# Optimization experiments

Measured on AMD Instinct MI355X. Metric: run time of the kernel, lower is better.

The kernel has to match this reference:

```python
import jax, jax.numpy as jnp
import numpy as np

N_NODES = 50000
N_EDGES = 800000
ND = 64
ED = 32
MSG = 128
HID = 256
N_AGENTS = 25000


def setup_inputs() -> dict:
    key = jax.random.key(0)
    ks = jax.random.split(key, 12)
    s = lambda k, shape, fan: jax.random.normal(k, shape, jnp.float32) / np.sqrt(fan)
    return {
        'node_feats': jax.random.normal(ks[0], (N_NODES, ND), jnp.float32),
        'edge_feats': jax.random.normal(ks[1], (N_EDGES, ED), jnp.float32),
        'W_msg1': s(ks[2], (2 * ND + ED, HID), 2 * ND + ED),
        'b_msg1': jnp.zeros((HID,), jnp.float32),
        'W_msg2': s(ks[3], (HID, MSG), HID),
        'b_msg2': jnp.zeros((MSG,), jnp.float32),
        'w_gate': s(ks[4], (MSG, 1), MSG),
        'b_gate': jnp.zeros((1,), jnp.float32),
        'W_h1': s(ks[5], (MSG, HID), MSG),
        'b_h1': jnp.zeros((HID,), jnp.float32),
        'W_h2': s(ks[6], (HID, HID), HID),
        'b_h2': jnp.zeros((HID,), jnp.float32),
        'W_out': s(ks[7], (HID, 1), HID),
        'b_out': jnp.zeros((1,), jnp.float32),
        'senders': jax.random.randint(ks[8], (N_EDGES,), 0, N_NODES, jnp.int32),
        'receivers': jax.random.randint(ks[9], (N_EDGES,), 0, N_NODES, jnp.int32),
        'n_agents': N_AGENTS,
    }


def reference(node_feats, edge_feats, W_msg1, b_msg1, W_msg2, b_msg2,
              w_gate, b_gate, W_h1, b_h1, W_h2, b_h2, W_out, b_out,
              senders, receivers, n_agents):
    n_nodes = node_feats.shape[0]
    # gather sender/receiver features, build edge messages (gather-transform)
    msg_in = jnp.concatenate(
        [node_feats[senders], node_feats[receivers], edge_feats], axis=-1)  # [E, 2*ND+ED]
    h = jax.nn.relu(msg_in @ W_msg1 + b_msg1)                               # [E, HID]
    msg = jax.nn.relu(h @ W_msg2 + b_msg2)                                  # [E, MSG]
    # per-receiver segment softmax attention
    logits = (msg @ w_gate + b_gate)[:, 0]                                  # [E]
    seg_max = jax.ops.segment_max(logits, receivers, num_segments=n_nodes)  # [N]
    e = jnp.exp(logits - seg_max[receivers])                                # [E]
    denom = jax.ops.segment_sum(e, receivers, num_segments=n_nodes)         # [N]
    attn = e / (denom[receivers] + 1e-9)                                    # [E]
    # scatter-aggregate messages to nodes
    aggr = jax.ops.segment_sum(attn[:, None] * msg, receivers,
                               num_segments=n_nodes)                        # [N, MSG]
    # node_type == 0: agent nodes are the first n_agents nodes
    x = aggr[:n_agents]                                                     # [A, MSG]
    # head MLP
    x = jax.nn.relu(x @ W_h1 + b_h1)
    x = jax.nn.relu(x @ W_h2 + b_h2)
    # Dense(1) + tanh
    return jnp.tanh(x @ W_out + b_out)                                      # [A, 1]
```

## Files before the change

### kernel.cpp

```cpp
#include <hip/hip_runtime.h>
#include <hip/hip_bf16.h>

#define N_NODES  50000
#define N_EDGES  800000
#define ND       64
#define ED       32
#define MSGD     128
#define HIDD     256
#define N_AGENTS 25000
#define EPAD     800064

typedef _Float16 f16;
typedef __attribute__((ext_vector_type(4))) _Float16 f16x4;
typedef __attribute__((ext_vector_type(8))) _Float16 f16x8;
typedef __attribute__((ext_vector_type(4))) float f32x4;
typedef unsigned short u16;
typedef unsigned int   u32;
typedef unsigned long long u64;

__global__ __launch_bounds__(256) void pack_weights(
    const float* __restrict__ W1, const float* __restrict__ W2,
    const float* __restrict__ Wh1, const float* __restrict__ Wh2,
    f16* __restrict__ F1, f16* __restrict__ F2,
    f16* __restrict__ F3, f16* __restrict__ F4)
{
    int tid  = blockIdx.x * 256 + threadIdx.x;
    int grp  = tid >> 6, lane = tid & 63;
    const float* W; f16* D; int NT, stride, gl;
    if      (grp < 80)  { W = W1;  D = F1; NT = 16; stride = 256; gl = grp; }
    else if (grp < 144) { W = W2;  D = F2; NT = 8;  stride = 128; gl = grp - 80; }
    else if (grp < 208) { W = Wh1; D = F3; NT = 16; stride = 256; gl = grp - 144; }
    else if (grp < 336) { W = Wh2; D = F4; NT = 16; stride = 256; gl = grp - 208; }
    else return;
    int ks = gl / NT, nt = gl - ks * NT;
    int n  = nt * 16 + (lane & 15);
    int k0 = ks * 32 + (lane >> 4) * 8;
    f16* dst = D + ((size_t)gl * 64 + lane) * 8;
    #pragma unroll
    for (int j = 0; j < 8; ++j)
        dst[j] = (f16)W[(size_t)(k0 + j) * stride + n];
}

__global__ __launch_bounds__(256) void compact_kernel(
    const int* __restrict__ recv, const float* __restrict__ nf,
    f16* __restrict__ nf16, int* __restrict__ rankb,
    int* __restrict__ deg)
{
    int i = blockIdx.x * 256 + threadIdx.x;
    {
        float4 v = ((const float4*)nf)[i];
        f16x4 h;
        h.x = (f16)v.x; h.y = (f16)v.y; h.z = (f16)v.z; h.w = (f16)v.w;
        ((f16x4*)nf16)[i] = h;
    }
    int r = recv[i];
    if (r < N_AGENTS)
        rankb[i] = atomicAdd(&deg[r], 1);
}

__global__ __launch_bounds__(1024) void prefix_kernel(
    const int* __restrict__ deg, int* __restrict__ off)
{
    __shared__ int part[1024];
    int t = threadIdx.x;
    int i0 = t * 25;
    int s = 0;
    #pragma unroll 1
    for (int i = 0; i < 25; ++i) {
        int idx = i0 + i;
        if (idx < N_AGENTS) s += deg[idx];
    }
    part[t] = s;
    __syncthreads();
    for (int d = 1; d < 1024; d <<= 1) {
        int v = (t >= d) ? part[t - d] : 0;
        __syncthreads();
        part[t] += v;
        __syncthreads();
    }
    int run = (t == 0) ? 0 : part[t - 1];
    #pragma unroll 1
    for (int i = 0; i < 25; ++i) {
        int idx = i0 + i;
        if (idx < N_AGENTS) {
            off[idx] = run;
            run += deg[idx];
        }
    }
    if (t == 1023) off[N_AGENTS] = part[1023];
}

__global__ __launch_bounds__(256) void scatter_kernel(
    const int* __restrict__ recv, const int* __restrict__ send,
    const int* __restrict__ rankb, const int* __restrict__ off,
    int* __restrict__ eidb, int* __restrict__ sendb, int* __restrict__ recvb)
{
    int i = blockIdx.x * 256 + threadIdx.x;
    int r = recv[i];
    if (r < N_AGENTS) {
        int pos = off[r] + rankb[i];
        eidb[pos]  = i;
        sendb[pos] = send[i];
        recvb[pos] = r;
    }
}

__global__ __launch_bounds__(512, 4) void edge_mlp_mfma(
    const f16* __restrict__ nf16, const float* __restrict__ ef,
    const f16* __restrict__ F1, const f16* __restrict__ F2,
    const float* __restrict__ b1, const float* __restrict__ b2,
    const float* __restrict__ wg, const float* __restrict__ bg,
    const int* __restrict__ sendb, const int* __restrict__ recvb,
    const int* __restrict__ eidb, const int* __restrict__ cnt,
    f16* __restrict__ msg_out, float* __restrict__ evals)
{
    __shared__ __align__(16) f16 XF[2][10][64][8];
    __shared__ __align__(16) f16 HB[16][64][8];
    __shared__ __align__(16) f16 msgt[32][136];
    __shared__ float lpart[8][32];

    const int tid  = threadIdx.x;
    const int wv   = tid >> 6;
    const int lane = tid & 63;
    const int q    = lane >> 4;
    const int li   = lane & 15;
    const int cntv   = cnt[0];
    const int ntiles = (cntv + 31) >> 5;

    const int xcd   = blockIdx.x & 7;
    const int bslot = blockIdx.x >> 3;
    const int tstep = gridDim.x >> 3;
    const int T8    = (ntiles + 7) >> 3;
    const int tend  = min((xcd + 1) * T8, ntiles);
    const int t0    = xcd * T8 + bslot;

    f16x8 w1[2][5], w2[8];
    #pragma unroll
    for (int ntl = 0; ntl < 2; ++ntl)
        #pragma unroll
        for (int ks = 0; ks < 5; ++ks)
            w1[ntl][ks] = *(const f16x8*)(F1 + (((size_t)(ks * 16 + 2 * wv + ntl)) * 64 + lane) * 8);
    #pragma unroll
    for (int ks = 0; ks < 8; ++ks)
        w2[ks] = *(const f16x8*)(F2 + (((size_t)(ks * 8 + wv)) * 64 + lane) * 8);

    const float4 ba  = *(const float4*)&b1[wv * 32 + q * 4];
    const float4 bb  = *(const float4*)&b1[wv * 32 + 16 + q * 4];
    const float4 bc  = *(const float4*)&b2[wv * 16 + q * 4];
    const float4 wg4 = *(const float4*)&wg[wv * 16 + q * 4];
    const float  bgv = bg[0];

    if (t0 < tend) {
        const int e0p = t0 * 32;
        f16 (*XFd)[64][8] = XF[0];
        for (int idx = tid; idx < 768; idx += 512) {
            int e = idx / 24, g = idx - e * 24;
            int cp = e0p + e;
            if (g < 16) {
                int node = (g < 8) ? sendb[cp] : recvb[cp];
                f16x8 h = *(const f16x8*)(nf16 + (size_t)node * 64 + (g & 7) * 8);
                int slt = (e >> 4) * 5 + (g >> 2);
                int ln  = (e & 15) + 16 * (g & 3);
                *(f16x8*)&XFd[slt][ln][0] = h;
            } else {
                int eid = eidb[cp];
                float4 v = ((const float4*)ef)[(size_t)eid * 8 + (g - 16)];
                int k0  = 128 + (g - 16) * 4;
                int slt = (e >> 4) * 5 + 4;
                int ln  = (e & 15) + 16 * ((k0 & 31) >> 3);
                int j0  = k0 & 7;
                f16x4 h;
                h.x = (f16)v.x; h.y = (f16)v.y; h.z = (f16)v.z; h.w = (f16)v.w;
                *(f16x4*)&XFd[slt][ln][j0] = h;
            }
        }
    }
    __syncthreads();

    int p = 0;
    for (int t = t0; t < tend; t += tstep) {
        const int e0 = t * 32;
        const int tn = t + tstep;

        if (tn < tend) {
            const int e0n = tn * 32;
            f16 (*XFd)[64][8] = XF[p ^ 1];
            for (int idx = tid; idx < 768; idx += 512) {
                int e = idx / 24, g = idx - e * 24;
                int cp = e0n + e;
                if (g < 16) {
                    int node = (g < 8) ? sendb[cp] : recvb[cp];
                    f16x8 h = *(const f16x8*)(nf16 + (size_t)node * 64 + (g & 7) * 8);
                    int slt = (e >> 4) * 5 + (g >> 2);
                    int ln  = (e & 15) + 16 * (g & 3);
                    *(f16x8*)&XFd[slt][ln][0] = h;
                } else {
                    int eid = eidb[cp];
                    float4 v = ((const float4*)ef)[(size_t)eid * 8 + (g - 16)];
                    int k0  = 128 + (g - 16) * 4;
                    int slt = (e >> 4) * 5 + 4;
                    int ln  = (e & 15) + 16 * ((k0 & 31) >> 3);
                    int j0  = k0 & 7;
                    f16x4 h;
                    h.x = (f16)v.x; h.y = (f16)v.y; h.z = (f16)v.z; h.w = (f16)v.w;
                    *(f16x4*)&XFd[slt][ln][j0] = h;
                }
            }
        }

        f32x4 acc[2][2];
        acc[0][0] = f32x4{ba.x, ba.y, ba.z, ba.w}; acc[1][0] = acc[0][0];
        acc[0][1] = f32x4{bb.x, bb.y, bb.z, bb.w}; acc[1][1] = acc[0][1];
        #pragma unroll
        for (int ks = 0; ks < 5; ++ks)
            #pragma unroll
            for (int eh = 0; eh < 2; ++eh) {
                f16x8 xh = *(const f16x8*)XF[p][eh * 5 + ks][lane];
                acc[eh][0] = __builtin_amdgcn_mfma_f32_16x16x32_f16(w1[0][ks], xh, acc[eh][0], 0, 0, 0);
                acc[eh][1] = __builtin_amdgcn_mfma_f32_16x16x32_f16(w1[1][ks], xh, acc[eh][1], 0, 0, 0);
            }
        #pragma unroll
        for (int eh = 0; eh < 2; ++eh)
            #pragma unroll
            for (int ntl = 0; ntl < 2; ++ntl) {
                f16x4 hv;
                hv.x = (f16)fmaxf(acc[eh][ntl][0], 0.f);
                hv.y = (f16)fmaxf(acc[eh][ntl][1], 0.f);
                hv.z = (f16)fmaxf(acc[eh][ntl][2], 0.f);
                hv.w = (f16)fmaxf(acc[eh][ntl][3], 0.f);
                int l2 = li + 16 * (2 * ntl + (q >> 1));
                int j0 = (q & 1) * 4;
                *(f16x4*)&HB[eh * 8 + wv][l2][j0] = hv;
            }
        __syncthreads();

        f32x4 acc2[2];
        acc2[0] = f32x4{bc.x, bc.y, bc.z, bc.w}; acc2[1] = acc2[0];
        #pragma unroll
        for (int ks2 = 0; ks2 < 8; ++ks2)
            #pragma unroll
            for (int eh = 0; eh < 2; ++eh) {
                f16x8 hh = *(const f16x8*)HB[eh * 8 + ks2][lane];
                acc2[eh] = __builtin_amdgcn_mfma_f32_16x16x32_f16(w2[ks2], hh, acc2[eh], 0, 0, 0);
            }
        {
            float pr[2];
            #pragma unroll
            for (int eh = 0; eh < 2; ++eh) {
                float v0 = fmaxf(acc2[eh][0], 0.f);
                float v1 = fmaxf(acc2[eh][1], 0.f);
                float v2 = fmaxf(acc2[eh][2], 0.f);
                float v3 = fmaxf(acc2[eh][3], 0.f);
                f16x4 mm;
                mm.x = (f16)v0; mm.y = (f16)v1; mm.z = (f16)v2; mm.w = (f16)v3;
                *(f16x4*)&msgt[eh * 16 + li][wv * 16 + q * 4] = mm;
                float pp = v0 * wg4.x + v1 * wg4.y + v2 * wg4.z + v3 * wg4.w;
                pp += __shfl_xor(pp, 16, 64);
                pp += __shfl_xor(pp, 32, 64);
                pr[eh] = pp;
            }
            if (lane < 16) {
                lpart[wv][li]      = pr[0];
                lpart[wv][16 + li] = pr[1];
            }
        }
        __syncthreads();

        {
            int row = tid >> 4, cg = tid & 15;
            *(uint4*)(msg_out + (size_t)(e0 + row) * 128 + cg * 8) =
                *(const uint4*)&msgt[row][cg * 8];
        }
        if (tid < 32) {
            float s2 = bgv;
            #pragma unroll
            for (int w = 0; w < 8; ++w) s2 += lpart[w][tid];
            evals[e0 + tid] = expf(s2);
        }
        p ^= 1;
    }
}

__global__ __launch_bounds__(1024, 4) void agg_agent_mfma(
    const int* __restrict__ off, const float* __restrict__ evals,
    const f16* __restrict__ msg,
    const f16* __restrict__ F3, const f16* __restrict__ F4,
    const float* __restrict__ bh1, const float* __restrict__ bh2,
    const float* __restrict__ Wout, const float* __restrict__ bout,
    float* __restrict__ out)
{
    __shared__ __align__(16) f16 XA[8][64][8];
    __shared__ __align__(16) f16 HB2[16][64][8];
    __shared__ float lpart[16][32];

    const int tid  = threadIdx.x;
    const int wv   = tid >> 6;
    const int lane = tid & 63;
    const int q    = lane >> 4;
    const int li   = lane & 15;
    const int a0i  = blockIdx.x * 32;

    {
        int g = tid >> 5, c = tid & 31;
        int r = a0i + g;
        float den = 1e-9f;
        float4 acc = make_float4(0.f, 0.f, 0.f, 0.f);
        if (r < N_AGENTS) {
            int beg = off[r], end = off[r + 1];
            const u64* mp = (const u64*)(msg + (size_t)beg * 128) + c;
            int pp = beg;
            for (; pp + 3 < end; pp += 4, mp += 128) {
                float e0 = evals[pp], e1 = evals[pp + 1];
                float e2 = evals[pp + 2], e3 = evals[pp + 3];
                u64 u0 = mp[0], u1 = mp[32], u2 = mp[64], u3 = mp[96];
                den += (e0 + e1) + (e2 + e3);
                union { u64 u; f16 h[4]; } c0, c1, c2, c3;
                c0.u = u0; c1.u = u1; c2.u = u2; c3.u = u3;
                acc.x = fmaf(e3, (float)c3.h[0], fmaf(e2, (float)c2.h[0],
                        fmaf(e1, (float)c1.h[0], fmaf(e0, (float)c0.h[0], acc.x))));
                acc.y = fmaf(e3, (float)c3.h[1], fmaf(e2, (float)c2.h[1],
                        fmaf(e1, (float)c1.h[1], fmaf(e0, (float)c0.h[1], acc.y))));
                acc.z = fmaf(e3, (float)c3.h[2], fmaf(e2, (float)c2.h[2],
                        fmaf(e1, (float)c1.h[2], fmaf(e0, (float)c0.h[2], acc.z))));
                acc.w = fmaf(e3, (float)c3.h[3], fmaf(e2, (float)c2.h[3],
                        fmaf(e1, (float)c1.h[3], fmaf(e0, (float)c0.h[3], acc.w))));
            }
            for (; pp < end; ++pp, mp += 32) {
                float e = evals[pp];
                den += e;
                union { u64 u; f16 h[4]; } cv; cv.u = *mp;
                acc.x = fmaf(e, (float)cv.h[0], acc.x);
                acc.y = fmaf(e, (float)cv.h[1], acc.y);
                acc.z = fmaf(e, (float)cv.h[2], acc.z);
                acc.w = fmaf(e, (float)cv.h[3], acc.w);
            }
        }
        float inv = 1.0f / den;
        int k0   = c * 4;
        int slot = (g >> 4) * 4 + (k0 >> 5);
        int ln   = (g & 15) + 16 * ((k0 & 31) >> 3);
        int j0   = k0 & 7;
        f16x4 h;
        h.x = (f16)(acc.x * inv); h.y = (f16)(acc.y * inv);
        h.z = (f16)(acc.z * inv); h.w = (f16)(acc.w * inv);
        *(f16x4*)&XA[slot][ln][j0] = h;
    }
    __syncthreads();

    f16x8 wh1[4], wh2[8];
    #pragma unroll
    for (int ks = 0; ks < 4; ++ks)
        wh1[ks] = *(const f16x8*)(F3 + (((size_t)(ks * 16 + wv)) * 64 + lane) * 8);
    #pragma unroll
    for (int ks = 0; ks < 8; ++ks)
        wh2[ks] = *(const f16x8*)(F4 + (((size_t)(ks * 16 + wv)) * 64 + lane) * 8);

    f32x4 acc[2] = {};
    #pragma unroll
    for (int ks = 0; ks < 4; ++ks)
        #pragma unroll
        for (int eh = 0; eh < 2; ++eh) {
            f16x8 xh = *(const f16x8*)XA[eh * 4 + ks][lane];
            acc[eh] = __builtin_amdgcn_mfma_f32_16x16x32_f16(wh1[ks], xh, acc[eh], 0, 0, 0);
        }
    {
        const float4 b1v = ((const float4*)bh1)[wv * 4 + q];
        #pragma unroll
        for (int eh = 0; eh < 2; ++eh) {
            f16x4 hv;
            hv.x = (f16)fmaxf(acc[eh][0] + b1v.x, 0.f);
            hv.y = (f16)fmaxf(acc[eh][1] + b1v.y, 0.f);
            hv.z = (f16)fmaxf(acc[eh][2] + b1v.z, 0.f);
            hv.w = (f16)fmaxf(acc[eh][3] + b1v.w, 0.f);
            int l2 = li + 16 * ((wv & 1) * 2 + (q >> 1));
            int j0 = (q & 1) * 4;
            *(f16x4*)&HB2[eh * 8 + (wv >> 1)][l2][j0] = hv;
        }
    }
    __syncthreads();

    f32x4 acc2[2] = {};
    #pragma unroll
    for (int ks2 = 0; ks2 < 8; ++ks2)
        #pragma unroll
        for (int eh = 0; eh < 2; ++eh) {
            f16x8 hh = *(const f16x8*)HB2[eh * 8 + ks2][lane];
            acc2[eh] = __builtin_amdgcn_mfma_f32_16x16x32_f16(wh2[ks2], hh, acc2[eh], 0, 0, 0);
        }
    {
        const float4 b2v = ((const float4*)bh2)[wv * 4 + q];
        const float4 wo4 = ((const float4*)Wout)[wv * 4 + q];
        float pr[2];
        #pragma unroll
        for (int eh = 0; eh < 2; ++eh) {
            float pp = fmaxf(acc2[eh][0] + b2v.x, 0.f) * wo4.x
                     + fmaxf(acc2[eh][1] + b2v.y, 0.f) * wo4.y
                     + fmaxf(acc2[eh][2] + b2v.z, 0.f) * wo4.z
                     + fmaxf(acc2[eh][3] + b2v.w, 0.f) * wo4.w;
            pp += __shfl_xor(pp, 16, 64);
            pp += __shfl_xor(pp, 32, 64);
            pr[eh] = pp;
        }
        if (lane < 16) {
            lpart[wv][li]      = pr[0];
            lpart[wv][16 + li] = pr[1];
        }
    }
    __syncthreads();

    if (tid < 32 && a0i + tid < N_AGENTS) {
        float s = bout[0];
        #pragma unroll
        for (int w = 0; w < 16; ++w) s += lpart[w][tid];
        out[a0i + tid] = tanhf(s);
    }
}

extern "C" void kernel_launch(void* const* d_in, const int* in_sizes, int n_in,
                              void* d_out, int out_size, void* d_ws, size_t ws_size,
                              hipStream_t stream)
{
    const float* nf   = (const float*)d_in[0];
    const float* ef   = (const float*)d_in[1];
    const float* W1   = (const float*)d_in[2];
    const float* b1   = (const float*)d_in[3];
    const float* W2   = (const float*)d_in[4];
    const float* b2   = (const float*)d_in[5];
    const float* wg   = (const float*)d_in[6];
    const float* bg   = (const float*)d_in[7];
    const float* Wh1  = (const float*)d_in[8];
    const float* bh1  = (const float*)d_in[9];
    const float* Wh2  = (const float*)d_in[10];
    const float* bh2  = (const float*)d_in[11];
    const float* Wout = (const float*)d_in[12];
    const float* bout = (const float*)d_in[13];
    const int*   send = (const int*)d_in[14];
    const int*   recv = (const int*)d_in[15];

    char* ws = (char*)d_ws;
    int* deg    = (int*)ws;            ws += (size_t)N_AGENTS * 4;
    int* eidb   = (int*)ws;            ws += (size_t)EPAD * 4;
    int* sendb  = (int*)ws;            ws += (size_t)EPAD * 4;
    int* recvb  = (int*)ws;            ws += (size_t)EPAD * 4;
    size_t zero_bytes = (size_t)(ws - (char*)d_ws);
    int* rankb  = (int*)ws;            ws += (size_t)N_EDGES * 4;
    int* off    = (int*)ws;            ws += (size_t)(N_AGENTS + 8) * 4;
    float* evals = (float*)ws;         ws += (size_t)EPAD * 4;
    f16* nf16   = (f16*)ws;            ws += (size_t)N_NODES * ND * 2;
    f16* F1     = (f16*)ws;            ws += (size_t)160 * 256 * 2;
    f16* F2     = (f16*)ws;            ws += (size_t)256 * 128 * 2;
    f16* F3     = (f16*)ws;            ws += (size_t)128 * 256 * 2;
    f16* F4     = (f16*)ws;            ws += (size_t)256 * 256 * 2;
    f16* msg    = (f16*)ws;

    hipMemsetAsync(d_ws, 0, zero_bytes, stream);

    pack_weights<<<84, 256, 0, stream>>>(W1, W2, Wh1, Wh2, F1, F2, F3, F4);
    compact_kernel<<<N_EDGES / 256, 256, 0, stream>>>(
        recv, nf, nf16, rankb, deg);
    prefix_kernel<<<1, 1024, 0, stream>>>(deg, off);
    scatter_kernel<<<N_EDGES / 256, 256, 0, stream>>>(
        recv, send, rankb, off, eidb, sendb, recvb);
    edge_mlp_mfma<<<512, 512, 0, stream>>>(
        nf16, ef, F1, F2, b1, b2, wg, bg, sendb, recvb, eidb, off + N_AGENTS, msg, evals);
    agg_agent_mfma<<<(N_AGENTS + 31) / 32, 1024, 0, stream>>>(
        off, evals, msg, F3, F4, bh1, bh2, Wout, bout, (float*)d_out);
}
```

Baseline: 415.8 us.

## Fuse weight packing into compact kernel, unroll aggregation by 8, enlarge edge grid

Merges the weight-packing kernel into the node-conversion/degree-count kernel as extra blocks, which removes one launch. Adds an 8-wide unrolled loop in the per-agent aggregation so more message loads are in flight per iteration. Raises the edge MLP grid from 512 to 768 blocks to change occupancy and load balance. The larger unroll raises register pressure, and the grid change assumes the edge kernel loops over its work with a grid stride.

```diff
diff --git a/kernel.cpp b/kernel.cpp
--- a/kernel.cpp
+++ b/kernel.cpp
@@ -18,35 +18,34 @@
 typedef unsigned int   u32;
 typedef unsigned long long u64;
 
-__global__ __launch_bounds__(256) void pack_weights(
+__global__ __launch_bounds__(256) void compact_pack_kernel(
+    const int* __restrict__ recv, const float* __restrict__ nf,
+    f16* __restrict__ nf16, int* __restrict__ rankb, int* __restrict__ deg,
     const float* __restrict__ W1, const float* __restrict__ W2,
     const float* __restrict__ Wh1, const float* __restrict__ Wh2,
     f16* __restrict__ F1, f16* __restrict__ F2,
     f16* __restrict__ F3, f16* __restrict__ F4)
 {
-    int tid  = blockIdx.x * 256 + threadIdx.x;
-    int grp  = tid >> 6, lane = tid & 63;
-    const float* W; f16* D; int NT, stride, gl;
-    if      (grp < 80)  { W = W1;  D = F1; NT = 16; stride = 256; gl = grp; }
-    else if (grp < 144) { W = W2;  D = F2; NT = 8;  stride = 128; gl = grp - 80; }
-    else if (grp < 208) { W = Wh1; D = F3; NT = 16; stride = 256; gl = grp - 144; }
-    else if (grp < 336) { W = Wh2; D = F4; NT = 16; stride = 256; gl = grp - 208; }
-    else return;
-    int ks = gl / NT, nt = gl - ks * NT;
-    int n  = nt * 16 + (lane & 15);
-    int k0 = ks * 32 + (lane >> 4) * 8;
-    f16* dst = D + ((size_t)gl * 64 + lane) * 8;
-    #pragma unroll
-    for (int j = 0; j < 8; ++j)
-        dst[j] = (f16)W[(size_t)(k0 + j) * stride + n];
-}
-
-__global__ __launch_bounds__(256) void compact_kernel(
-    const int* __restrict__ recv, const float* __restrict__ nf,
-    f16* __restrict__ nf16, int* __restrict__ rankb,
-    int* __restrict__ deg)
-{
-    int i = blockIdx.x * 256 + threadIdx.x;
+    int b = blockIdx.x;
+    if (b >= N_EDGES / 256) {
+        int tid  = (b - N_EDGES / 256) * 256 + threadIdx.x;
+        int grp  = tid >> 6, lane = tid & 63;
+        const float* W; f16* D; int NT, stride, gl;
+        if      (grp < 80)  { W = W1;  D = F1; NT = 16; stride = 256; gl = grp; }
+        else if (grp < 144) { W = W2;  D = F2; NT = 8;  stride = 128; gl = grp - 80; }
+        else if (grp < 208) { W = Wh1; D = F3; NT = 16; stride = 256; gl = grp - 144; }
+        else if (grp < 336) { W = Wh2; D = F4; NT = 16; stride = 256; gl = grp - 208; }
+        else return;
+        int ks = gl / NT, nt = gl - ks * NT;
+        int n  = nt * 16 + (lane & 15);
+        int k0 = ks * 32 + (lane >> 4) * 8;
+        f16* dst = D + ((size_t)gl * 64 + lane) * 8;
+        #pragma unroll
+        for (int j = 0; j < 8; ++j)
+            dst[j] = (f16)W[(size_t)(k0 + j) * stride + n];
+        return;
+    }
+    int i = b * 256 + threadIdx.x;
     {
         float4 v = ((const float4*)nf)[i];
         f16x4 h;
@@ -309,6 +308,36 @@
             int beg = off[r], end = off[r + 1];
             const u64* mp = (const u64*)(msg + (size_t)beg * 128) + c;
             int pp = beg;
+            for (; pp + 7 < end; pp += 8, mp += 256) {
+                float e0 = evals[pp],     e1 = evals[pp + 1];
+                float e2 = evals[pp + 2], e3 = evals[pp + 3];
+                float e4 = evals[pp + 4], e5 = evals[pp + 5];
+                float e6 = evals[pp + 6], e7 = evals[pp + 7];
+                u64 u0 = mp[0],   u1 = mp[32],  u2 = mp[64],  u3 = mp[96];
+                u64 u4 = mp[128], u5 = mp[160], u6 = mp[192], u7 = mp[224];
+                den += ((e0 + e1) + (e2 + e3)) + ((e4 + e5) + (e6 + e7));
+                union { u64 u; f16 h[4]; } c0, c1, c2, c3, c4, c5, c6, c7;
+                c0.u = u0; c1.u = u1; c2.u = u2; c3.u = u3;
+                c4.u = u4; c5.u = u5; c6.u = u6; c7.u = u7;
+                #pragma unroll
+                for (int k = 0; k < 1; ++k) { }
+                acc.x = fmaf(e3, (float)c3.h[0], fmaf(e2, (float)c2.h[0],
+                        fmaf(e1, (float)c1.h[0], fmaf(e0, (float)c0.h[0], acc.x))));
+                acc.y = fmaf(e3, (float)c3.h[1], fmaf(e2, (float)c2.h[1],
+                        fmaf(e1, (float)c1.h[1], fmaf(e0, (float)c0.h[1], acc.y))));
+                acc.z = fmaf(e3, (float)c3.h[2], fmaf(e2, (float)c2.h[2],
+                        fmaf(e1, (float)c1.h[2], fmaf(e0, (float)c0.h[2], acc.z))));
+                acc.w = fmaf(e3, (float)c3.h[3], fmaf(e2, (float)c2.h[3],
+                        fmaf(e1, (float)c1.h[3], fmaf(e0, (float)c0.h[3], acc.w))));
+                acc.x = fmaf(e7, (float)c7.h[0], fmaf(e6, (float)c6.h[0],
+                        fmaf(e5, (float)c5.h[0], fmaf(e4, (float)c4.h[0], acc.x))));
+                acc.y = fmaf(e7, (float)c7.h[1], fmaf(e6, (float)c6.h[1],
+                        fmaf(e5, (float)c5.h[1], fmaf(e4, (float)c4.h[1], acc.y))));
+                acc.z = fmaf(e7, (float)c7.h[2], fmaf(e6, (float)c6.h[2],
+                        fmaf(e5, (float)c5.h[2], fmaf(e4, (float)c4.h[2], acc.z))));
+                acc.w = fmaf(e7, (float)c7.h[3], fmaf(e6, (float)c6.h[3],
+                        fmaf(e5, (float)c5.h[3], fmaf(e4, (float)c4.h[3], acc.w))));
+            }
             for (; pp + 3 < end; pp += 4, mp += 128) {
                 float e0 = evals[pp], e1 = evals[pp + 1];
                 float e2 = evals[pp + 2], e3 = evals[pp + 3];
@@ -455,13 +484,12 @@
 
     hipMemsetAsync(d_ws, 0, zero_bytes, stream);
 
-    pack_weights<<<84, 256, 0, stream>>>(W1, W2, Wh1, Wh2, F1, F2, F3, F4);
-    compact_kernel<<<N_EDGES / 256, 256, 0, stream>>>(
-        recv, nf, nf16, rankb, deg);
+    compact_pack_kernel<<<N_EDGES / 256 + 84, 256, 0, stream>>>(
+        recv, nf, nf16, rankb, deg, W1, W2, Wh1, Wh2, F1, F2, F3, F4);
     prefix_kernel<<<1, 1024, 0, stream>>>(deg, off);
     scatter_kernel<<<N_EDGES / 256, 256, 0, stream>>>(
         recv, send, rankb, off, eidb, sendb, recvb);
-    edge_mlp_mfma<<<512, 512, 0, stream>>>(
+    edge_mlp_mfma<<<768, 512, 0, stream>>>(
         nf16, ef, F1, F2, b1, b2, wg, bg, sendb, recvb, eidb, off + N_AGENTS, msg, evals);
     agg_agent_mfma<<<(N_AGENTS + 31) / 32, 1024, 0, stream>>>(
         off, evals, msg, F3, F4, bh1, bh2, Wout, bout, (float*)d_out);
```

Result: slower. 450.3 us (+8.3%).
